# Performance work log

Measured on AMD Instinct MI355X. Metric: run time of the kernel, lower is better.

## Reference

```python
import jax, jax.numpy as jnp
import numpy as np

N, K, W = 500000, 512, 64


def setup_inputs() -> dict:
    key = jax.random.key(0)
    kx, kc = jax.random.split(key)
    X = jax.random.normal(kx, (N, W), dtype=jnp.float32)
    # nn.init.uniform_(codebook.weight, a=-1.0, b=1.0)
    codebook = jax.random.uniform(kc, (K, W), dtype=jnp.float32, minval=-1.0, maxval=1.0)
    return {"X": X, "codebook": codebook}


def reference(X, codebook):
    # torch.cdist (p=2): pairwise Euclidean distances [N, K]
    x2 = jnp.sum(X * X, axis=-1, keepdims=True)          # [N, 1]
    c2 = jnp.sum(codebook * codebook, axis=-1)           # [K]
    d2 = x2 - 2.0 * (X @ codebook.T) + c2[None, :]        # [N, K]
    dist = jnp.sqrt(jnp.maximum(d2, 0.0))
    idx = jnp.argmin(dist, axis=-1)                       # [N] int
    min_dists = jnp.min(dist, axis=-1)                    # [N] == gather(dist, idx)
    return idx, min_dists
```

## Files before the change

kernel.cpp:

```cpp
#include <hip/hip_runtime.h>

#define N_POINTS 500000
#define K_CENT   512
#define W_DIM    64
#define N_SUB    (N_POINTS / 16)
#define N_JOBS   ((N_SUB + 2) / 3)

typedef _Float16 half8 __attribute__((ext_vector_type(8)));
typedef float    f32x4 __attribute__((ext_vector_type(4)));

__global__ void cvt_kernel(const float* __restrict__ cb,
                           _Float16* __restrict__ cbf) {
    int id = blockIdx.x * 256 + threadIdx.x;
    if (id >= K_CENT * 8) return;
    int c = id >> 3, o = (id & 7) * 8;
    int t = c >> 5, csub = (c >> 4) & 1, r = c & 15;
    int kstep = o >> 5, grp = (o >> 3) & 3;
    int lane = grp * 16 + r;
    const float* src = cb + (size_t)c * W_DIM + o;
    half8 h, l;
#pragma unroll
    for (int j = 0; j < 8; ++j) {
        float w = -2.0f * src[j];
        _Float16 hh = (_Float16)w;
        h[j] = hh;
        l[j] = (_Float16)(w - (float)hh);
    }
    size_t bh = ((((size_t)t * 2 + 0) * 2 + csub) * 2 + kstep) * 512 + (size_t)lane * 8;
    size_t bl = ((((size_t)t * 2 + 1) * 2 + csub) * 2 + kstep) * 512 + (size_t)lane * 8;
    *(half8*)(cbf + bh) = h;
    *(half8*)(cbf + bl) = l;
}

__global__ void c2_kernel(const float* __restrict__ cb, float* __restrict__ c2) {
    int c = blockIdx.x * 256 + threadIdx.x;
    if (c >= K_CENT) return;
    const float4* row = (const float4*)(cb + (size_t)c * W_DIM);
    double s = 0.0;
#pragma unroll
    for (int j = 0; j < W_DIM / 4; ++j) {
        float4 v = row[j];
        s += (double)v.x * v.x + (double)v.y * v.y + (double)v.z * v.z + (double)v.w * v.w;
    }
    c2[c] = (float)s;
}

#define MFMA16(A, B, C) __builtin_amdgcn_mfma_f32_16x16x32_f16(A, B, C, 0, 0, 0)

#define PREFETCH_A(T, DH, DL)                                                  \
    {                                                                          \
        const _Float16* nb = cbf + (size_t)(T) * 4096 + (size_t)lane * 8;      \
        DH[0][0] = *(const half8*)(nb + 0 * 512);                              \
        DH[0][1] = *(const half8*)(nb + 1 * 512);                              \
        DH[1][0] = *(const half8*)(nb + 2 * 512);                              \
        DH[1][1] = *(const half8*)(nb + 3 * 512);                              \
        DL[0][0] = *(const half8*)(nb + 2048 + 0 * 512);                       \
        DL[0][1] = *(const half8*)(nb + 2048 + 1 * 512);                       \
        DL[1][0] = *(const half8*)(nb + 2048 + 2 * 512);                       \
        DL[1][1] = *(const half8*)(nb + 2048 + 3 * 512);                       \
    }

#define CHUNK(T, AH, AL, NXH, NXL)                                             \
    {                                                                          \
        int t_ = (T);                                                          \
        if (t_ < 15) { PREFETCH_A(t_ + 1, NXH, NXL) }                          \
        _Pragma("unroll")                                                      \
        for (int cs = 0; cs < 2; ++cs) {                                       \
            _Pragma("unroll")                                                  \
            for (int ps = 0; ps < 3; ++ps)                                     \
                accA[cs][ps] = MFMA16(AH[cs][0], bh[ps][0], cs ? q1 : q0);     \
        }                                                                      \
        _Pragma("unroll")                                                      \
        for (int cs = 0; cs < 2; ++cs) {                                       \
            _Pragma("unroll")                                                  \
            for (int ps = 0; ps < 3; ++ps)                                     \
                accB[cs][ps] = MFMA16(AH[cs][1], bh[ps][1], zro4);             \
        }                                                                      \
        _Pragma("unroll")                                                      \
        for (int cs = 0; cs < 2; ++cs) {                                       \
            _Pragma("unroll")                                                  \
            for (int ps = 0; ps < 3; ++ps)                                     \
                accA[cs][ps] = MFMA16(AL[cs][0], bh[ps][0], accA[cs][ps]);     \
        }                                                                      \
        _Pragma("unroll")                                                      \
        for (int cs = 0; cs < 2; ++cs) {                                       \
            _Pragma("unroll")                                                  \
            for (int ps = 0; ps < 3; ++ps)                                     \
                accB[cs][ps] = MFMA16(AL[cs][1], bh[ps][1], accB[cs][ps]);     \
        }                                                                      \
        _Pragma("unroll")                                                      \
        for (int cs = 0; cs < 2; ++cs) {                                       \
            _Pragma("unroll")                                                  \
            for (int ps = 0; ps < 3; ++ps)                                     \
                accA[cs][ps] = MFMA16(AH[cs][0], bl[ps][0], accA[cs][ps]);     \
        }                                                                      \
        _Pragma("unroll")                                                      \
        for (int cs = 0; cs < 2; ++cs) {                                       \
            _Pragma("unroll")                                                  \
            for (int ps = 0; ps < 3; ++ps)                                     \
                accB[cs][ps] = MFMA16(AH[cs][1], bl[ps][1], accB[cs][ps]);     \
        }                                                                      \
        if (t_ < 15) {                                                         \
            q0 = *(const f32x4*)&c2s[(t_ + 1) * 32 + 0 * 16 + grp4];           \
            q1 = *(const f32x4*)&c2s[(t_ + 1) * 32 + 1 * 16 + grp4];           \
        }                                                                      \
        _Pragma("unroll")                                                      \
        for (int ps = 0; ps < 3; ++ps) {                                       \
            float v0 = accA[0][ps][0] + accB[0][ps][0];                        \
            float v1 = accA[0][ps][1] + accB[0][ps][1];                        \
            float v2 = accA[0][ps][2] + accB[0][ps][2];                        \
            float v3 = accA[0][ps][3] + accB[0][ps][3];                        \
            float v4 = accA[1][ps][0] + accB[1][ps][0];                        \
            float v5 = accA[1][ps][1] + accB[1][ps][1];                        \
            float v6 = accA[1][ps][2] + accB[1][ps][2];                        \
            float v7 = accA[1][ps][3] + accB[1][ps][3];                        \
            float a0 = fminf(v0, v1), a1 = fminf(v2, v3);                      \
            float a2 = fminf(v4, v5), a3 = fminf(v6, v7);                      \
            float b0 = fminf(a0, a1), b1 = fminf(a2, a3);                      \
            float m  = fminf(b0, b1);                                          \
            bool  L2 = (m == b0);                                              \
            float aL = L2 ? a0 : a2;                                           \
            bool  L1 = (m == aL);                                              \
            float vE = L2 ? (L1 ? v0 : v2) : (L1 ? v4 : v6);                   \
            bool  L0 = (m == vE);                                              \
            int ji = (L2 ? 0 : 4) | (L1 ? 0 : 2) | (L0 ? 0 : 1);               \
            int ci = t_ * 32 + (ji >> 2) * 16 + grp4 + (ji & 3);               \
            bool imp = m < bd[ps];                                             \
            bd[ps] = imp ? m : bd[ps];                                         \
            bi[ps] = imp ? ci : bi[ps];                                        \
        }                                                                      \
    }

__global__ __launch_bounds__(256, 2)
void kmeans_mfma(const float* __restrict__ X,
                 const _Float16* __restrict__ cbf,
                 const float* __restrict__ c2,
                 float* __restrict__ out_idx,
                 float* __restrict__ out_dist) {
    __shared__ __align__(16) float c2s[K_CENT];
    int tid = threadIdx.x;
    c2s[tid] = c2[tid];
    c2s[tid + 256] = c2[tid + 256];
    __syncthreads();

    int wave = tid >> 6;
    int lane = tid & 63;
    int l15  = lane & 15;
    int grp  = lane >> 4;
    int grp4 = grp * 4;
    int grp8 = grp * 8;

    int job = blockIdx.x * 4 + wave;
    if (job >= N_JOBS) return;
    int sub0 = job * 3;

    half8 bh[3][2], bl[3][2];
    float x2[3] = {0.f, 0.f, 0.f};
#pragma unroll
    for (int ps = 0; ps < 3; ++ps) {
        int p = (sub0 + ps) * 16 + l15;
        int pe = p < N_POINTS ? p : (N_POINTS - 1);
#pragma unroll
        for (int ks = 0; ks < 2; ++ks) {
            const float4* xp = (const float4*)(X + (size_t)pe * W_DIM + ks * 32 + grp8);
            float4 f0 = xp[0], f1 = xp[1];
            float fa[8] = {f0.x, f0.y, f0.z, f0.w, f1.x, f1.y, f1.z, f1.w};
#pragma unroll
            for (int j = 0; j < 8; ++j) {
                _Float16 hh = (_Float16)fa[j];
                bh[ps][ks][j] = hh;
                bl[ps][ks][j] = (_Float16)(fa[j] - (float)hh);
                x2[ps] = fmaf(fa[j], fa[j], x2[ps]);
            }
        }
    }
#pragma unroll
    for (int ps = 0; ps < 3; ++ps) {
        x2[ps] += __shfl_xor(x2[ps], 16);
        x2[ps] += __shfl_xor(x2[ps], 32);
    }

    float bd[3] = {3.4e38f, 3.4e38f, 3.4e38f};
    int   bi[3] = {0, 0, 0};

    f32x4 zro4 = {0.f, 0.f, 0.f, 0.f};
    f32x4 q0, q1;
    f32x4 accA[2][3], accB[2][3];
    half8 ahA[2][2], alA[2][2], ahB[2][2], alB[2][2];

    PREFETCH_A(0, ahA, alA)
    q0 = *(const f32x4*)&c2s[0 * 16 + grp4];
    q1 = *(const f32x4*)&c2s[1 * 16 + grp4];

#pragma unroll 1
    for (int tt = 0; tt < 8; ++tt) {
        CHUNK(2 * tt,     ahA, alA, ahB, alB)
        CHUNK(2 * tt + 1, ahB, alB, ahA, alA)
    }

#pragma unroll
    for (int ps = 0; ps < 3; ++ps) {
        float od = __shfl_xor(bd[ps], 16); int oi = __shfl_xor(bi[ps], 16);
        if (od < bd[ps] || (od == bd[ps] && oi < bi[ps])) { bd[ps] = od; bi[ps] = oi; }
        od = __shfl_xor(bd[ps], 32); oi = __shfl_xor(bi[ps], 32);
        if (od < bd[ps] || (od == bd[ps] && oi < bi[ps])) { bd[ps] = od; bi[ps] = oi; }
    }

    if (grp == 0) {
#pragma unroll
        for (int ps = 0; ps < 3; ++ps) {
            int p = (sub0 + ps) * 16 + l15;
            if (p < N_POINTS) {
                out_idx[p]  = (float)bi[ps];
                out_dist[p] = sqrtf(fmaxf(bd[ps] + x2[ps], 0.f));
            }
        }
    }
}

extern "C" void kernel_launch(void* const* d_in, const int* in_sizes, int n_in,
                              void* d_out, int out_size, void* d_ws, size_t ws_size,
                              hipStream_t stream) {
    const float* X  = (const float*)d_in[0];
    const float* cb = (const float*)d_in[1];
    float* out      = (float*)d_out;

    _Float16* cbf = (_Float16*)d_ws;
    float*    c2  = (float*)(cbf + (size_t)K_CENT * W_DIM * 2);

    hipLaunchKernelGGL(cvt_kernel, dim3((K_CENT * 8 + 255) / 256), dim3(256), 0, stream, cb, cbf);
    hipLaunchKernelGGL(c2_kernel, dim3((K_CENT + 255) / 256), dim3(256), 0, stream, cb, c2);

    hipLaunchKernelGGL(kmeans_mfma, dim3((N_JOBS + 3) / 4), dim3(256), 0, stream,
                       X, cbf, c2, out, out + N_POINTS);
}
```

Measured before the change: 113.0 us.

## Software-pipeline MFMA chunks with argmin reduction using double accumulators

```diff
diff --git a/kernel.cpp b/kernel.cpp
--- a/kernel.cpp
+++ b/kernel.cpp
@@ -60,60 +60,54 @@
         DL[1][1] = *(const half8*)(nb + 2048 + 3 * 512);                       \
     }
 
-#define CHUNK(T, AH, AL, NXH, NXL)                                             \
+#define MFMA_CHUNK(T, AH, AL, NXH, NXL, ACC)                                   \
     {                                                                          \
         int t_ = (T);                                                          \
         if (t_ < 15) { PREFETCH_A(t_ + 1, NXH, NXL) }                          \
         _Pragma("unroll")                                                      \
-        for (int cs = 0; cs < 2; ++cs) {                                       \
-            _Pragma("unroll")                                                  \
-            for (int ps = 0; ps < 3; ++ps)                                     \
-                accA[cs][ps] = MFMA16(AH[cs][0], bh[ps][0], cs ? q1 : q0);     \
-        }                                                                      \
-        _Pragma("unroll")                                                      \
-        for (int cs = 0; cs < 2; ++cs) {                                       \
-            _Pragma("unroll")                                                  \
-            for (int ps = 0; ps < 3; ++ps)                                     \
-                accB[cs][ps] = MFMA16(AH[cs][1], bh[ps][1], zro4);             \
-        }                                                                      \
-        _Pragma("unroll")                                                      \
-        for (int cs = 0; cs < 2; ++cs) {                                       \
-            _Pragma("unroll")                                                  \
-            for (int ps = 0; ps < 3; ++ps)                                     \
-                accA[cs][ps] = MFMA16(AL[cs][0], bh[ps][0], accA[cs][ps]);     \
-        }                                                                      \
-        _Pragma("unroll")                                                      \
-        for (int cs = 0; cs < 2; ++cs) {                                       \
-            _Pragma("unroll")                                                  \
-            for (int ps = 0; ps < 3; ++ps)                                     \
-                accB[cs][ps] = MFMA16(AL[cs][1], bh[ps][1], accB[cs][ps]);     \
-        }                                                                      \
-        _Pragma("unroll")                                                      \
-        for (int cs = 0; cs < 2; ++cs) {                                       \
-            _Pragma("unroll")                                                  \
-            for (int ps = 0; ps < 3; ++ps)                                     \
-                accA[cs][ps] = MFMA16(AH[cs][0], bl[ps][0], accA[cs][ps]);     \
-        }                                                                      \
-        _Pragma("unroll")                                                      \
-        for (int cs = 0; cs < 2; ++cs) {                                       \
-            _Pragma("unroll")                                                  \
-            for (int ps = 0; ps < 3; ++ps)                                     \
-                accB[cs][ps] = MFMA16(AH[cs][1], bl[ps][1], accB[cs][ps]);     \
-        }                                                                      \
+        for (int cs = 0; cs < 2; ++cs)                                         \
+            _Pragma("unroll")                                                  \
+            for (int ps = 0; ps < 3; ++ps)                                     \
+                ACC[cs][ps] = MFMA16(AH[cs][0], bh[ps][0], cs ? q1 : q0);      \
+        _Pragma("unroll")                                                      \
+        for (int cs = 0; cs < 2; ++cs)                                         \
+            _Pragma("unroll")                                                  \
+            for (int ps = 0; ps < 3; ++ps)                                     \
+                ACC[cs][ps] = MFMA16(AH[cs][1], bh[ps][1], ACC[cs][ps]);       \
+        _Pragma("unroll")                                                      \
+        for (int cs = 0; cs < 2; ++cs)                                         \
+            _Pragma("unroll")                                                  \
+            for (int ps = 0; ps < 3; ++ps)                                     \
+                ACC[cs][ps] = MFMA16(AL[cs][0], bh[ps][0], ACC[cs][ps]);       \
+        _Pragma("unroll")                                                      \
+        for (int cs = 0; cs < 2; ++cs)                                         \
+            _Pragma("unroll")                                                  \
+            for (int ps = 0; ps < 3; ++ps)                                     \
+                ACC[cs][ps] = MFMA16(AL[cs][1], bh[ps][1], ACC[cs][ps]);       \
+        _Pragma("unroll")                                                      \
+        for (int cs = 0; cs < 2; ++cs)                                         \
+            _Pragma("unroll")                                                  \
+            for (int ps = 0; ps < 3; ++ps)                                     \
+                ACC[cs][ps] = MFMA16(AH[cs][0], bl[ps][0], ACC[cs][ps]);       \
+        _Pragma("unroll")                                                      \
+        for (int cs = 0; cs < 2; ++cs)                                         \
+            _Pragma("unroll")                                                  \
+            for (int ps = 0; ps < 3; ++ps)                                     \
+                ACC[cs][ps] = MFMA16(AH[cs][1], bl[ps][1], ACC[cs][ps]);       \
         if (t_ < 15) {                                                         \
             q0 = *(const f32x4*)&c2s[(t_ + 1) * 32 + 0 * 16 + grp4];           \
             q1 = *(const f32x4*)&c2s[(t_ + 1) * 32 + 1 * 16 + grp4];           \
         }                                                                      \
+    }
+
+#define ARGMIN_CHUNK(T_, ACC)                                                  \
+    {                                                                          \
         _Pragma("unroll")                                                      \
         for (int ps = 0; ps < 3; ++ps) {                                       \
-            float v0 = accA[0][ps][0] + accB[0][ps][0];                        \
-            float v1 = accA[0][ps][1] + accB[0][ps][1];                        \
-            float v2 = accA[0][ps][2] + accB[0][ps][2];                        \
-            float v3 = accA[0][ps][3] + accB[0][ps][3];                        \
-            float v4 = accA[1][ps][0] + accB[1][ps][0];                        \
-            float v5 = accA[1][ps][1] + accB[1][ps][1];                        \
-            float v6 = accA[1][ps][2] + accB[1][ps][2];                        \
-            float v7 = accA[1][ps][3] + accB[1][ps][3];                        \
+            float v0 = ACC[0][ps][0], v1 = ACC[0][ps][1];                      \
+            float v2 = ACC[0][ps][2], v3 = ACC[0][ps][3];                      \
+            float v4 = ACC[1][ps][0], v5 = ACC[1][ps][1];                      \
+            float v6 = ACC[1][ps][2], v7 = ACC[1][ps][3];                      \
             float a0 = fminf(v0, v1), a1 = fminf(v2, v3);                      \
             float a2 = fminf(v4, v5), a3 = fminf(v6, v7);                      \
             float b0 = fminf(a0, a1), b1 = fminf(a2, a3);                      \
@@ -124,7 +118,7 @@
             float vE = L2 ? (L1 ? v0 : v2) : (L1 ? v4 : v6);                   \
             bool  L0 = (m == vE);                                              \
             int ji = (L2 ? 0 : 4) | (L1 ? 0 : 2) | (L0 ? 0 : 1);               \
-            int ci = t_ * 32 + (ji >> 2) * 16 + grp4 + (ji & 3);               \
+            int ci = (T_) * 32 + (ji >> 2) * 16 + grp4 + (ji & 3);             \
             bool imp = m < bd[ps];                                             \
             bd[ps] = imp ? m : bd[ps];                                         \
             bi[ps] = imp ? ci : bi[ps];                                        \
@@ -183,20 +177,26 @@
     float bd[3] = {3.4e38f, 3.4e38f, 3.4e38f};
     int   bi[3] = {0, 0, 0};
 
-    f32x4 zro4 = {0.f, 0.f, 0.f, 0.f};
     f32x4 q0, q1;
-    f32x4 accA[2][3], accB[2][3];
+    f32x4 accP[2][3], accQ[2][3];
     half8 ahA[2][2], alA[2][2], ahB[2][2], alB[2][2];
 
     PREFETCH_A(0, ahA, alA)
     q0 = *(const f32x4*)&c2s[0 * 16 + grp4];
     q1 = *(const f32x4*)&c2s[1 * 16 + grp4];
 
+    MFMA_CHUNK(0, ahA, alA, ahB, alB, accP)
+
 #pragma unroll 1
-    for (int tt = 0; tt < 8; ++tt) {
-        CHUNK(2 * tt,     ahA, alA, ahB, alB)
-        CHUNK(2 * tt + 1, ahB, alB, ahA, alA)
-    }
+    for (int tt = 0; tt < 7; ++tt) {
+        MFMA_CHUNK(2 * tt + 1, ahB, alB, ahA, alA, accQ)
+        ARGMIN_CHUNK(2 * tt, accP)
+        MFMA_CHUNK(2 * tt + 2, ahA, alA, ahB, alB, accP)
+        ARGMIN_CHUNK(2 * tt + 1, accQ)
+    }
+    MFMA_CHUNK(15, ahB, alB, ahA, alA, accQ)
+    ARGMIN_CHUNK(14, accP)
+    ARGMIN_CHUNK(15, accQ)
 
 #pragma unroll
     for (int ps = 0; ps < 3; ++ps) {
```

New measurement: 104.0 us. -7.9%, faster.
